# Kernel tuning notes

Hardware: AMD Instinct MI355X
Metric: run time of the kernel (lower is better)

## Reference

```python
import jax, jax.numpy as jnp
import numpy as np

EPS = 1e-12  # torch F.normalize eps
ALPHA = 100.0


def _l2norm(v, axis):
    n = jnp.sqrt(jnp.sum(v * v, axis=axis, keepdims=True))
    return v / jnp.maximum(n, EPS)


def setup_inputs() -> dict:
    key = jax.random.key(0)
    kx, kc = jax.random.split(key)
    B, D, H, W, K = 16, 512, 64, 64, 64
    x = jax.random.normal(kx, (B, D, H, W), dtype=jnp.float32)
    centroids = jax.random.uniform(kc, (K, D), dtype=jnp.float32)
    # NetVLAD._init_params: conv weight/bias derived from centroids at init
    conv_w = 2.0 * ALPHA * centroids                 # [K, D] (1x1 conv kernel)
    conv_b = -ALPHA * jnp.linalg.norm(centroids, axis=1)  # [K]
    return {"x": x, "centroids": centroids, "conv_w": conv_w, "conv_b": conv_b}


def reference(x, centroids, conv_w, conv_b):
    B, D = x.shape[:2]
    K = centroids.shape[0]
    # descriptor-wise L2 normalization over channel dim
    x = _l2norm(x, axis=1)
    xf = x.reshape(B, D, -1)                          # [B, D, N]
    # 1x1 conv == per-position matmul: [B, K, N]
    logits = jnp.einsum('kd,bdn->bkn', conv_w, xf) + conv_b[None, :, None]
    assign = jax.nn.softmax(logits, axis=1)           # soft assignment over K
    # vlad[b,k,d] = sum_n a[b,k,n]*(x[b,d,n] - c[k,d])
    #            = (a @ x^T) - a.sum(n) * c   (avoids B*K*D*N intermediate)
    agg = jnp.einsum('bkn,bdn->bkd', assign, xf)      # [B, K, D]
    mass = jnp.sum(assign, axis=-1)                   # [B, K]
    vlad = agg - mass[..., None] * centroids[None]    # [B, K, D]
    vlad = _l2norm(vlad, axis=2)                      # intra-normalization
    vlad = vlad.reshape(B, -1)                        # [B, K*D]
    return _l2norm(vlad, axis=1)
```

## Files before the change

kernel.cpp:

```cpp
#include <hip/hip_runtime.h>
#include <cstddef>

constexpr int Bn = 16, Dn = 512, Nn = 4096, Kn = 64;
constexpr float FEPS = 1e-12f;

typedef __bf16 bf16x8 __attribute__((ext_vector_type(8)));
typedef float f32x4 __attribute__((ext_vector_type(4)));

__device__ __forceinline__ unsigned short bf_bits(__bf16 h) {
  union { __bf16 b; unsigned short u; } c;
  c.b = h;
  return c.u;
}

__global__ __launch_bounds__(256) void kW(const float* __restrict__ w,
                                          unsigned short* __restrict__ w_hi,
                                          unsigned short* __restrict__ w_lo) {
  const int idx = blockIdx.x * 256 + threadIdx.x;
  const float v = w[idx];
  const __bf16 h = (__bf16)v;
  const float r = v - (float)h;
  const __bf16 l = (__bf16)r;
  w_hi[idx] = bf_bits(h);
  w_lo[idx] = bf_bits(l);
}

__global__ __launch_bounds__(1024) void kF(const float* __restrict__ x,
                                           const unsigned short* __restrict__ w_hi,
                                           const unsigned short* __restrict__ w_lo,
                                           const float* __restrict__ conv_b,
                                           float* __restrict__ aggp,
                                           float* __restrict__ massp) {
  __shared__ float smem[2 * 256 * 33];
  __shared__ float msum[16][64];
  const int tid = threadIdx.x;
  const int l = tid & 63;
  const int wv = tid >> 6;
  const int ll = l & 15;
  const int lg = l >> 4;
  const int b = blockIdx.x >> 4;
  const int p = blockIdx.x & 15;
  const int n0 = p << 8;
  const float* xb = x + (size_t)b * Dn * Nn + n0;

  f32x4 acc[4];
#pragma unroll
  for (int kt = 0; kt < 4; ++kt) acc[kt] = (f32x4){0.f, 0.f, 0.f, 0.f};
  float ss = 0.f;

  float pf[2][4];
#pragma unroll
  for (int i = 0; i < 2; ++i)
#pragma unroll
    for (int q = 0; q < 4; ++q)
      pf[i][q] = xb[(size_t)(wv + 16 * i) * Nn + l + 64 * q];

  for (int dc = 0; dc < Dn; dc += 32) {
    float* xs = smem + ((dc >> 5) & 1) * (256 * 33);
#pragma unroll
    for (int i = 0; i < 2; ++i)
#pragma unroll
      for (int q = 0; q < 4; ++q)
        xs[(l + 64 * q) * 33 + wv + 16 * i] = pf[i][q];
    if (dc + 32 < Dn) {
#pragma unroll
      for (int i = 0; i < 2; ++i)
#pragma unroll
        for (int q = 0; q < 4; ++q)
          pf[i][q] = xb[(size_t)(dc + 32 + wv + 16 * i) * Nn + l + 64 * q];
    }
    __syncthreads();

    const int ncol = (wv << 4) + ll;
    float xv[8];
#pragma unroll
    for (int j = 0; j < 8; ++j) xv[j] = xs[ncol * 33 + lg * 8 + j];
    bf16x8 bh, bl;
#pragma unroll
    for (int j = 0; j < 8; ++j) {
      ss = fmaf(xv[j], xv[j], ss);
      const __bf16 h = (__bf16)xv[j];
      bh[j] = h;
      bl[j] = (__bf16)(xv[j] - (float)h);
    }
#pragma unroll
    for (int kt = 0; kt < 4; ++kt) {
      const size_t woff = (size_t)(kt * 16 + ll) * Dn + dc + lg * 8;
      bf16x8 ah = *(const bf16x8*)(w_hi + woff);
      bf16x8 al = *(const bf16x8*)(w_lo + woff);
      acc[kt] = __builtin_amdgcn_mfma_f32_16x16x32_bf16(ah, bh, acc[kt], 0, 0, 0);
      acc[kt] = __builtin_amdgcn_mfma_f32_16x16x32_bf16(ah, bl, acc[kt], 0, 0, 0);
      acc[kt] = __builtin_amdgcn_mfma_f32_16x16x32_bf16(al, bh, acc[kt], 0, 0, 0);
    }
  }

  ss += __shfl_xor(ss, 16);
  ss += __shfl_xor(ss, 32);
  const float iv = 1.f / fmaxf(sqrtf(ss), FEPS);
  float lgt[16];
#pragma unroll
  for (int kt = 0; kt < 4; ++kt)
#pragma unroll
    for (int r = 0; r < 4; ++r)
      lgt[kt * 4 + r] = fmaf(acc[kt][r], iv, conv_b[kt * 16 + lg * 4 + r]);
  float pmax = lgt[0];
#pragma unroll
  for (int i = 1; i < 16; ++i) pmax = fmaxf(pmax, lgt[i]);
  pmax = fmaxf(pmax, __shfl_xor(pmax, 16));
  pmax = fmaxf(pmax, __shfl_xor(pmax, 32));
  float ex[16];
  float psum = 0.f;
#pragma unroll
  for (int i = 0; i < 16; ++i) {
    ex[i] = expf(lgt[i] - pmax);
    psum += ex[i];
  }
  psum += __shfl_xor(psum, 16);
  psum += __shfl_xor(psum, 32);
  const float isum = 1.f / psum;

  __syncthreads();

  unsigned short* as_hi = (unsigned short*)smem;
  unsigned short* as_lo = as_hi + 16384;
  const int ngb = (wv << 1) + (ll >> 3);
  const int jj = ll & 7;
#pragma unroll
  for (int i = 0; i < 16; ++i) {
    const int k = (i >> 2) * 16 + lg * 4 + (i & 3);
    const float a = ex[i] * isum;
    const float v = a * iv;
    const __bf16 h = (__bf16)v;
    as_hi[(ngb * 64 + k) * 8 + jj] = bf_bits(h);
    as_lo[(ngb * 64 + k) * 8 + jj] = bf_bits((__bf16)(v - (float)h));
    float m = a;
    m += __shfl_xor(m, 1);
    m += __shfl_xor(m, 2);
    m += __shfl_xor(m, 4);
    m += __shfl_xor(m, 8);
    if (ll == 0) msum[wv][k] = m;
  }
  __syncthreads();
  if (tid < 64) {
    float s = 0.f;
#pragma unroll
    for (int ww = 0; ww < 16; ++ww) s += msum[ww][tid];
    massp[((b << 4) + p) * Kn + tid] = s;
  }

  f32x4 acc2[4][2];
#pragma unroll
  for (int kt = 0; kt < 4; ++kt)
#pragma unroll
    for (int dt = 0; dt < 2; ++dt) acc2[kt][dt] = (f32x4){0.f, 0.f, 0.f, 0.f};

  const float* xq0 = x + (size_t)b * Dn * Nn +
                     (size_t)(wv * 32 + ll) * Nn + n0 + lg * 8;
  const float* xq1 = xq0 + (size_t)16 * Nn;

#pragma unroll 2
  for (int nc = 0; nc < 256; nc += 32) {
    const int ng = (nc >> 3) + lg;
    bf16x8 af_h[4], af_l[4];
#pragma unroll
    for (int kt = 0; kt < 4; ++kt) {
      const int idx = (ng * 64 + kt * 16 + ll) * 8;
      af_h[kt] = *(const bf16x8*)(as_hi + idx);
      af_l[kt] = *(const bf16x8*)(as_lo + idx);
    }
    bf16x8 bx[2];
#pragma unroll
    for (int dt = 0; dt < 2; ++dt) {
      const float* xr = (dt == 0 ? xq0 : xq1) + nc;
      float4 x0 = *(const float4*)(xr);
      float4 x1 = *(const float4*)(xr + 4);
      bx[dt][0] = (__bf16)x0.x; bx[dt][1] = (__bf16)x0.y;
      bx[dt][2] = (__bf16)x0.z; bx[dt][3] = (__bf16)x0.w;
      bx[dt][4] = (__bf16)x1.x; bx[dt][5] = (__bf16)x1.y;
      bx[dt][6] = (__bf16)x1.z; bx[dt][7] = (__bf16)x1.w;
    }
#pragma unroll
    for (int kt = 0; kt < 4; ++kt)
#pragma unroll
      for (int dt = 0; dt < 2; ++dt) {
        acc2[kt][dt] =
            __builtin_amdgcn_mfma_f32_16x16x32_bf16(af_h[kt], bx[dt], acc2[kt][dt], 0, 0, 0);
        acc2[kt][dt] =
            __builtin_amdgcn_mfma_f32_16x16x32_bf16(af_l[kt], bx[dt], acc2[kt][dt], 0, 0, 0);
      }
  }

  float* outb = aggp + ((size_t)((b << 4) + p) * Kn) * Dn;
#pragma unroll
  for (int kt = 0; kt < 4; ++kt)
#pragma unroll
    for (int dt = 0; dt < 2; ++dt) {
      const int krow = kt * 16 + (lg << 2);
      const int dcol = wv * 32 + dt * 16 + ll;
      float* op = outb + (size_t)krow * Dn + dcol;
#pragma unroll
      for (int r = 0; r < 4; ++r) op[(size_t)r * Dn] = acc2[kt][dt][r];
    }
}

__device__ __forceinline__ float blockReduceSum(float v, float* sb) {
#pragma unroll
  for (int off = 32; off > 0; off >>= 1) v += __shfl_down(v, off, 64);
  const int lane = threadIdx.x & 63, w = threadIdx.x >> 6;
  if (lane == 0) sb[w] = v;
  __syncthreads();
  if (threadIdx.x == 0) sb[4] = sb[0] + sb[1] + sb[2] + sb[3];
  __syncthreads();
  return sb[4];
}

__global__ __launch_bounds__(256) void kC1(const float* __restrict__ massp,
                                           const float* __restrict__ aggp,
                                           const float* __restrict__ centroids,
                                           float* __restrict__ out,
                                           float* __restrict__ rowsq) {
  __shared__ float sb[5];
  const int tid = threadIdx.x;
  const int b = blockIdx.x >> 6, k = blockIdx.x & 63;
  float s = 0.f;
  if (tid < 16) s = massp[((b << 4) + tid) * Kn + k];
  const float mass = blockReduceSum(s, sb);
  float v[2];
  float sq = 0.f;
#pragma unroll
  for (int u = 0; u < 2; ++u) {
    const int d = tid + (u << 8);
    float val = -mass * centroids[k * Dn + d];
#pragma unroll
    for (int pp = 0; pp < 16; ++pp)
      val += aggp[((size_t)((b << 4) + pp) * Kn + k) * Dn + d];
    v[u] = val;
    sq = fmaf(val, val, sq);
  }
  const float rsq = blockReduceSum(sq, sb);
  const float inv = 1.f / fmaxf(sqrtf(rsq), FEPS);
#pragma unroll
  for (int u = 0; u < 2; ++u)
    out[((size_t)b * Kn + k) * Dn + tid + (u << 8)] = v[u] * inv;
  if (tid == 0) rowsq[b * Kn + k] = rsq * inv * inv;
}

__global__ __launch_bounds__(256) void kC2(float* __restrict__ out,
                                           const float* __restrict__ rowsq) {
  __shared__ float sg;
  const int b = blockIdx.x, tid = threadIdx.x;
  float v = (tid < 64) ? rowsq[b * Kn + tid] : 0.f;
  if (tid < 64) {
#pragma unroll
    for (int off = 32; off > 0; off >>= 1) v += __shfl_down(v, off, 64);
  }
  if (tid == 0) sg = 1.f / fmaxf(sqrtf(v), FEPS);
  __syncthreads();
  const float inv = sg;
  float* ob = out + (size_t)b * (Kn * Dn);
  for (int t = tid; t < Kn * Dn; t += 256) ob[t] *= inv;
}

extern "C" void kernel_launch(void* const* d_in, const int* in_sizes, int n_in,
                              void* d_out, int out_size, void* d_ws,
                              size_t ws_size, hipStream_t stream) {
  const float* x = (const float*)d_in[0];
  const float* centroids = (const float*)d_in[1];
  const float* conv_w = (const float*)d_in[2];
  const float* conv_b = (const float*)d_in[3];
  float* out = (float*)d_out;
  float* ws = (float*)d_ws;
  float* aggp = ws;
  unsigned short* w_hi = (unsigned short*)(ws + 8388608);
  unsigned short* w_lo = (unsigned short*)(ws + 8404992);
  float* massp = ws + 8421376;
  float* rowsq = ws + 8437760;

  kW<<<128, 256, 0, stream>>>(conv_w, w_hi, w_lo);
  kF<<<256, 1024, 0, stream>>>(x, w_hi, w_lo, conv_b, aggp, massp);
  kC1<<<1024, 256, 0, stream>>>(massp, aggp, centroids, out, rowsq);
  kC2<<<16, 256, 0, stream>>>(out, rowsq);
}
```

Baseline: 136.1 us.

## Split spatial dimension into 128-column partitions with 512-thread blocks and padded partials

The fused assignment/aggregation kernel now processes 128 spatial positions per block with 8 waves instead of 256 positions with 16 waves. That doubles the grid to 512 blocks, and each wave now covers 64 descriptor channels in the second GEMM. Global loads of x switch to float4 per thread, and the partial aggregate rows are padded to 520 floats to reduce bank or channel conflicts. The cost is twice as many partial sums for the combine kernel to reduce, so the workspace and kC1 traffic both double.

Result: slower. 143.4 us (+5.3%).

```diff
diff --git a/kernel.cpp b/kernel.cpp
--- a/kernel.cpp
+++ b/kernel.cpp
@@ -2,6 +2,9 @@
 #include <cstddef>
 
 constexpr int Bn = 16, Dn = 512, Nn = 4096, Kn = 64;
+constexpr int PN = 128;
+constexpr int NP = Nn / PN;
+constexpr int Dp = 520;
 constexpr float FEPS = 1e-12f;
 
 typedef __bf16 bf16x8 __attribute__((ext_vector_type(8)));
@@ -25,22 +28,22 @@
   w_lo[idx] = bf_bits(l);
 }
 
-__global__ __launch_bounds__(1024) void kF(const float* __restrict__ x,
-                                           const unsigned short* __restrict__ w_hi,
-                                           const unsigned short* __restrict__ w_lo,
-                                           const float* __restrict__ conv_b,
-                                           float* __restrict__ aggp,
-                                           float* __restrict__ massp) {
-  __shared__ float smem[2 * 256 * 33];
-  __shared__ float msum[16][64];
+__global__ __launch_bounds__(512, 4) void kF(const float* __restrict__ x,
+                                             const unsigned short* __restrict__ w_hi,
+                                             const unsigned short* __restrict__ w_lo,
+                                             const float* __restrict__ conv_b,
+                                             float* __restrict__ aggp,
+                                             float* __restrict__ massp) {
+  __shared__ float smem[2 * PN * 33];
+  __shared__ float msum[8][64];
   const int tid = threadIdx.x;
   const int l = tid & 63;
   const int wv = tid >> 6;
   const int ll = l & 15;
   const int lg = l >> 4;
-  const int b = blockIdx.x >> 4;
-  const int p = blockIdx.x & 15;
-  const int n0 = p << 8;
+  const int b = blockIdx.x >> 5;
+  const int p = blockIdx.x & 31;
+  const int n0 = p << 7;
   const float* xb = x + (size_t)b * Dn * Nn + n0;
 
   f32x4 acc[4];
@@ -48,33 +51,32 @@
   for (int kt = 0; kt < 4; ++kt) acc[kt] = (f32x4){0.f, 0.f, 0.f, 0.f};
   float ss = 0.f;
 
-  float pf[2][4];
-#pragma unroll
-  for (int i = 0; i < 2; ++i)
-#pragma unroll
-    for (int q = 0; q < 4; ++q)
-      pf[i][q] = xb[(size_t)(wv + 16 * i) * Nn + l + 64 * q];
+  const int srow = tid >> 4;
+  const int sc0 = (tid & 15) << 3;
+  float4 pf0 = *(const float4*)(xb + (size_t)srow * Nn + sc0);
+  float4 pf1 = *(const float4*)(xb + (size_t)srow * Nn + sc0 + 4);
 
   for (int dc = 0; dc < Dn; dc += 32) {
-    float* xs = smem + ((dc >> 5) & 1) * (256 * 33);
-#pragma unroll
-    for (int i = 0; i < 2; ++i)
-#pragma unroll
-      for (int q = 0; q < 4; ++q)
-        xs[(l + 64 * q) * 33 + wv + 16 * i] = pf[i][q];
+    float* xs = smem + ((dc >> 5) & 1) * (PN * 33);
+    xs[(sc0 + 0) * 33 + srow] = pf0.x;
+    xs[(sc0 + 1) * 33 + srow] = pf0.y;
+    xs[(sc0 + 2) * 33 + srow] = pf0.z;
+    xs[(sc0 + 3) * 33 + srow] = pf0.w;
+    xs[(sc0 + 4) * 33 + srow] = pf1.x;
+    xs[(sc0 + 5) * 33 + srow] = pf1.y;
+    xs[(sc0 + 6) * 33 + srow] = pf1.z;
+    xs[(sc0 + 7) * 33 + srow] = pf1.w;
     if (dc + 32 < Dn) {
-#pragma unroll
-      for (int i = 0; i < 2; ++i)
-#pragma unroll
-        for (int q = 0; q < 4; ++q)
-          pf[i][q] = xb[(size_t)(dc + 32 + wv + 16 * i) * Nn + l + 64 * q];
+      pf0 = *(const float4*)(xb + (size_t)(dc + 32 + srow) * Nn + sc0);
+      pf1 = *(const float4*)(xb + (size_t)(dc + 32 + srow) * Nn + sc0 + 4);
     }
     __syncthreads();
 
     const int ncol = (wv << 4) + ll;
+    const float* xcol = xs + ncol * 33 + lg * 8;
     float xv[8];
 #pragma unroll
-    for (int j = 0; j < 8; ++j) xv[j] = xs[ncol * 33 + lg * 8 + j];
+    for (int j = 0; j < 8; ++j) xv[j] = xcol[j];
     bf16x8 bh, bl;
 #pragma unroll
     for (int j = 0; j < 8; ++j) {
@@ -122,7 +124,7 @@
   __syncthreads();
 
   unsigned short* as_hi = (unsigned short*)smem;
-  unsigned short* as_lo = as_hi + 16384;
+  unsigned short* as_lo = as_hi + PN * Kn;
   const int ngb = (wv << 1) + (ll >> 3);
   const int jj = ll & 7;
 #pragma unroll
@@ -144,22 +146,21 @@
   if (tid < 64) {
     float s = 0.f;
 #pragma unroll
-    for (int ww = 0; ww < 16; ++ww) s += msum[ww][tid];
-    massp[((b << 4) + p) * Kn + tid] = s;
-  }
-
-  f32x4 acc2[4][2];
+    for (int ww = 0; ww < 8; ++ww) s += msum[ww][tid];
+    massp[((b << 5) + p) * Kn + tid] = s;
+  }
+
+  f32x4 acc2[4][4];
 #pragma unroll
   for (int kt = 0; kt < 4; ++kt)
 #pragma unroll
-    for (int dt = 0; dt < 2; ++dt) acc2[kt][dt] = (f32x4){0.f, 0.f, 0.f, 0.f};
-
-  const float* xq0 = x + (size_t)b * Dn * Nn +
-                     (size_t)(wv * 32 + ll) * Nn + n0 + lg * 8;
-  const float* xq1 = xq0 + (size_t)16 * Nn;
-
-#pragma unroll 2
-  for (int nc = 0; nc < 256; nc += 32) {
+    for (int dt = 0; dt < 4; ++dt) acc2[kt][dt] = (f32x4){0.f, 0.f, 0.f, 0.f};
+
+  const float* xq = x + (size_t)b * Dn * Nn +
+                    (size_t)(wv * 64 + ll) * Nn + n0 + lg * 8;
+
+#pragma unroll
+  for (int nc = 0; nc < PN; nc += 32) {
     const int ng = (nc >> 3) + lg;
     bf16x8 af_h[4], af_l[4];
 #pragma unroll
@@ -168,10 +169,10 @@
       af_h[kt] = *(const bf16x8*)(as_hi + idx);
       af_l[kt] = *(const bf16x8*)(as_lo + idx);
     }
-    bf16x8 bx[2];
-#pragma unroll
-    for (int dt = 0; dt < 2; ++dt) {
-      const float* xr = (dt == 0 ? xq0 : xq1) + nc;
+    bf16x8 bx[4];
+#pragma unroll
+    for (int dt = 0; dt < 4; ++dt) {
+      const float* xr = xq + (size_t)(dt * 16) * Nn + nc;
       float4 x0 = *(const float4*)(xr);
       float4 x1 = *(const float4*)(xr + 4);
       bx[dt][0] = (__bf16)x0.x; bx[dt][1] = (__bf16)x0.y;
@@ -182,24 +183,24 @@
 #pragma unroll
     for (int kt = 0; kt < 4; ++kt)
 #pragma unroll
-      for (int dt = 0; dt < 2; ++dt) {
-        acc2[kt][dt] =
-            __builtin_amdgcn_mfma_f32_16x16x32_bf16(af_h[kt], bx[dt], acc2[kt][dt], 0, 0, 0);
-        acc2[kt][dt] =
-            __builtin_amdgcn_mfma_f32_16x16x32_bf16(af_l[kt], bx[dt], acc2[kt][dt], 0, 0, 0);
+      for (int dt = 0; dt < 4; ++dt) {
+        acc2[kt][dt] = __builtin_amdgcn_mfma_f32_16x16x32_bf16(
+            af_h[kt], bx[dt], acc2[kt][dt], 0, 0, 0);
+        acc2[kt][dt] = __builtin_amdgcn_mfma_f32_16x16x32_bf16(
+            af_l[kt], bx[dt], acc2[kt][dt], 0, 0, 0);
       }
   }
 
-  float* outb = aggp + ((size_t)((b << 4) + p) * Kn) * Dn;
+  float* outb = aggp + (size_t)((b << 5) + p) * Kn * Dp;
 #pragma unroll
   for (int kt = 0; kt < 4; ++kt)
 #pragma unroll
-    for (int dt = 0; dt < 2; ++dt) {
+    for (int dt = 0; dt < 4; ++dt) {
       const int krow = kt * 16 + (lg << 2);
-      const int dcol = wv * 32 + dt * 16 + ll;
-      float* op = outb + (size_t)krow * Dn + dcol;
-#pragma unroll
-      for (int r = 0; r < 4; ++r) op[(size_t)r * Dn] = acc2[kt][dt][r];
+      const int dcol = wv * 64 + dt * 16 + ll;
+      float* op = outb + (size_t)krow * Dp + dcol;
+#pragma unroll
+      for (int r = 0; r < 4; ++r) op[(size_t)r * Dp] = acc2[kt][dt][r];
     }
 }
 
@@ -223,7 +224,7 @@
   const int tid = threadIdx.x;
   const int b = blockIdx.x >> 6, k = blockIdx.x & 63;
   float s = 0.f;
-  if (tid < 16) s = massp[((b << 4) + tid) * Kn + k];
+  if (tid < 32) s = massp[((b << 5) + tid) * Kn + k];
   const float mass = blockReduceSum(s, sb);
   float v[2];
   float sq = 0.f;
@@ -231,9 +232,9 @@
   for (int u = 0; u < 2; ++u) {
     const int d = tid + (u << 8);
     float val = -mass * centroids[k * Dn + d];
-#pragma unroll
-    for (int pp = 0; pp < 16; ++pp)
-      val += aggp[((size_t)((b << 4) + pp) * Kn + k) * Dn + d];
+#pragma unroll 8
+    for (int pp = 0; pp < 32; ++pp)
+      val += aggp[((size_t)((b << 5) + pp) * Kn + k) * Dp + d];
     v[u] = val;
     sq = fmaf(val, val, sq);
   }
@@ -271,13 +272,13 @@
   float* out = (float*)d_out;
   float* ws = (float*)d_ws;
   float* aggp = ws;
-  unsigned short* w_hi = (unsigned short*)(ws + 8388608);
-  unsigned short* w_lo = (unsigned short*)(ws + 8404992);
-  float* massp = ws + 8421376;
-  float* rowsq = ws + 8437760;
+  unsigned short* w_hi = (unsigned short*)(ws + 17039360);
+  unsigned short* w_lo = (unsigned short*)(ws + 17055744);
+  float* massp = ws + 17072128;
+  float* rowsq = ws + 17104896;
 
   kW<<<128, 256, 0, stream>>>(conv_w, w_hi, w_lo);
-  kF<<<256, 1024, 0, stream>>>(x, w_hi, w_lo, conv_b, aggp, massp);
+  kF<<<512, 512, 0, stream>>>(x, w_hi, w_lo, conv_b, aggp, massp);
   kC1<<<1024, 256, 0, stream>>>(massp, aggp, centroids, out, rowsq);
   kC2<<<16, 256, 0, stream>>>(out, rowsq);
 }
```
